# Optimization experiments

Hardware: AMD Instinct MI355X
Metric: run time of the kernel (lower is better)

## Reference

```python
import jax, jax.numpy as jnp
import numpy as np

EMBED, HID, INSIDE, OUTSIDE, EPS = 128, 64, 4, 8, 1e-5
N_NODES, N_EDGES, BATCH, SEQLEN = 16384, 262144, 64, 21


def _layernorm(x, g, b):
    m = x.mean(-1, keepdims=True)
    v = ((x - m) ** 2).mean(-1, keepdims=True)
    return (x - m) * jax.lax.rsqrt(v + EPS) * g + b


def _lstm_dir(x, Wih, Whh, bih, bhh, reverse):
    # x: [B, L, D] -> h: [B, L, HID]; PyTorch gate order i,f,g,o
    pre = jnp.einsum('bld,gd->blg', x, Wih) + bih + bhh  # [B,L,4H]
    pre = jnp.swapaxes(pre, 0, 1)  # [L,B,4H]
    h0 = jnp.zeros((x.shape[0], HID), x.dtype)

    def step(carry, xt):
        h, c = carry
        gates = xt + h @ Whh.T
        i, f, g, o = jnp.split(gates, 4, axis=-1)
        c = jax.nn.sigmoid(f) * c + jax.nn.sigmoid(i) * jnp.tanh(g)
        h = jax.nn.sigmoid(o) * jnp.tanh(c)
        return (h, c), h

    _, hs = jax.lax.scan(step, (h0, h0), pre, reverse=reverse)
    return jnp.swapaxes(hs, 0, 1)


def setup_inputs():
    key = jax.random.key(0)
    ks = jax.random.split(key, 40)
    f = jnp.float32
    N, E, B, L, D = N_NODES, N_EDGES, BATCH, SEQLEN, EMBED

    def w(k, shape, fan_in):
        return jax.random.normal(k, shape, f) * (1.0 / np.sqrt(fan_in))

    inp = {
        'x': jax.random.normal(ks[0], (N, 2561), f),
        'edge_index': jax.random.randint(ks[1], (2, E), 0, N, jnp.int32),
        'edge_attr': jax.random.normal(ks[2], (E, 3), f),
        # sorted node->graph assignment; every graph id 0..B-1 present
        'batch': ((jnp.arange(N, dtype=jnp.int32) * B) // N).astype(jnp.int32),
        'hotslice': jax.random.normal(ks[3], (B, L, 28), f),
        # randn_like noise tensors from the torch forward, made explicit inputs
        'noise_seqy': jax.random.normal(ks[4], (B, L, D), f),
        'noise_seqz': jax.random.normal(ks[5], (B, L, D), f),
        'noise_sty': jax.random.normal(ks[6], (N, D), f),
        'noise_stz': jax.random.normal(ks[7], (N, D), f),
        # AttnNN params
        'W_esm': w(ks[8], (D, 2560), 2560), 'b_esm': jnp.zeros((D,), f),
        'W_node': w(ks[9], (D, D + 1), D + 1), 'b_node': jnp.zeros((D,), f),
        'W_seq': w(ks[10], (D, 28), 28), 'b_seq': jnp.zeros((D,), f),
        # SeqStructBlock params
        'ln_seq_g': jnp.ones((D,), f), 'ln_seq_b': jnp.zeros((D,), f),
        'ln_st_g': jnp.ones((D,), f), 'ln_st_b': jnp.zeros((D,), f),
        'W_in': w(ks[11], (D, 2 * D + 3), 2 * D + 3), 'b_in': jnp.zeros((D,), f),
        'W_out': w(ks[12], (D, 2 * D + 3), 2 * D + 3), 'b_out': jnp.zeros((D,), f),
        'Wih_f': w(ks[13], (4 * HID, D), HID), 'Whh_f': w(ks[14], (4 * HID, HID), HID),
        'bih_f': jnp.zeros((4 * HID,), f), 'bhh_f': jnp.zeros((4 * HID,), f),
        'Wih_b': w(ks[15], (4 * HID, D), HID), 'Whh_b': w(ks[16], (4 * HID, HID), HID),
        'bih_b': jnp.zeros((4 * HID,), f), 'bhh_b': jnp.zeros((4 * HID,), f),
        # BatchNorm1d (eval mode: running stats)
        'bn_g': jnp.ones((D,), f), 'bn_b': jnp.zeros((D,), f),
        'bn_rm': jnp.zeros((D,), f), 'bn_rv': jnp.ones((D,), f),
    }
    return inp


def reference(x, edge_index, edge_attr, batch, hotslice,
              noise_seqy, noise_seqz, noise_sty, noise_stz,
              W_esm, b_esm, W_node, b_node, W_seq, b_seq,
              ln_seq_g, ln_seq_b, ln_st_g, ln_st_b,
              W_in, b_in, W_out, b_out,
              Wih_f, Whh_f, bih_f, bhh_f, Wih_b, Whh_b, bih_b, bhh_b,
              bn_g, bn_b, bn_rm, bn_rv):
    N = x.shape[0]
    B = hotslice.shape[0]
    src, dst = edge_index[0, 0::2], edge_index[1, 0::2]
    ea_in, ea_out = edge_attr[1::2], edge_attr[0::2]

    def ss(seq, struct):
        # bidirectional LSTM + residual + LayerNorm (dropout = identity, eval)
        hf = _lstm_dir(seq, Wih_f, Whh_f, bih_f, bhh_f, False)
        hb = _lstm_dir(seq, Wih_b, Whh_b, bih_b, bhh_b, True)
        seq = _layernorm(seq + jnp.concatenate([hf, hb], -1), ln_seq_g, ln_seq_b)
        sn = struct
        fs, fd = sn[src], sn[dst]  # [E/2, 128] gathers
        gin = jax.nn.sigmoid(jnp.concatenate([fs, fd, ea_in], -1) @ W_in.T + b_in)
        struct = struct + jax.ops.segment_sum(gin * fd, src, num_segments=N)
        gout = jax.nn.sigmoid(jnp.concatenate([fs, fd, ea_out], -1) @ W_out.T + b_out)
        struct = struct + jax.ops.segment_sum(gout * fs, dst, num_segments=N)
        return seq, _layernorm(struct, ln_st_g, ln_st_b)

    seq0 = hotslice @ W_seq.T + b_seq                       # [B,L,128]
    esm = x[:, 1:] @ W_esm.T + b_esm                        # [N,128]
    struct0 = jnp.concatenate([esm, x[:, :1]], -1) @ W_node.T + b_node  # [N,128]

    def outer(carry):
        sy, sz, ty, tz = carry

        def inner(c, _):
            szc, tzc = c
            return ss(seq0 + sy + szc, struct0 + ty + tzc), None

        (sz, tz), _ = jax.lax.scan(inner, (sz, tz), None, length=INSIDE)
        sy, ty = ss(sy + sz, ty + tz)
        return (sy, sz, ty, tz)

    carry = (noise_seqy, noise_seqz, noise_sty, noise_stz)
    carry, _ = jax.lax.scan(lambda c, _: (outer(c), None), carry, None,
                            length=OUTSIDE - 1)
    sy, sz, ty, tz = outer(carry)

    # middleSelect picks the first node of each consecutive batch run;
    # batch is sorted with every graph id present -> run starts via searchsorted
    starts = jnp.searchsorted(batch, jnp.arange(B, dtype=batch.dtype))
    feat = sy[:, 10, :] + ty[starts]                        # [B,128]
    # BatchNorm1d, eval mode (running stats)
    return (feat - bn_rm) * jax.lax.rsqrt(bn_rv + EPS) * bn_g + bn_b
```

## Files before the change

kernel.cpp:

```cpp
#include <hip/hip_runtime.h>
#include <hip/hip_fp16.h>
#include <math.h>

#define D 128
#define G4 256
#define LSEQ 21
#define EPSF 1e-5f

typedef unsigned short u16;
typedef __attribute__((ext_vector_type(8))) short bf16x8;
typedef __attribute__((ext_vector_type(4))) float f32x4;
typedef __attribute__((ext_vector_type(2))) unsigned u32x2;
typedef __attribute__((ext_vector_type(4))) unsigned u32x4;

#define MFMA16(a,b,c) __builtin_amdgcn_mfma_f32_16x16x32_bf16(a,b,c,0,0,0)

__device__ __forceinline__ float sigf(float x){ return 1.0f/(1.0f+__expf(-x)); }
__device__ __forceinline__ u16 f2bf(float x){
  unsigned u = __float_as_uint(x);
  return (u16)((u + 0x7FFFu + ((u>>16)&1u)) >> 16);
}
__device__ __forceinline__ float bf2f(u16 h){ return __uint_as_float(((unsigned)h)<<16); }
__device__ __forceinline__ unsigned pack_h2(float a, float b){
  __half2 h = __floats2half2_rn(a, b);
  return *(unsigned*)&h;
}
__device__ __forceinline__ float2 unpack_h2(unsigned u){
  __half2 h = *(__half2*)&u;
  return __half22float2(h);
}
__device__ __forceinline__ u16 f2h(float v){ __half h = __float2half(v); return *(u16*)&h; }

__device__ __forceinline__ void edge_acc(u32x4 a, uint2 g, bool valid,
                                         float2 po2, float2 w0, float2 w1, float2 w2,
                                         float& ax, float& ay){
  float e0=__uint_as_float(a.y), e1=__uint_as_float(a.z), e2=__uint_as_float(a.w);
  float2 ps0 = unpack_h2(g.x);
  float2 ps1 = unpack_h2(g.y);
  float gx = po2.x + ps0.x + e0*w0.x + e1*w1.x + e2*w2.x;
  float gy = po2.y + ps1.x + e0*w0.y + e1*w1.y + e2*w2.y;
  float mm = valid ? 1.f : 0.f;
  ax = fmaf(ps0.y*mm, sigf(gx), ax);
  ay = fmaf(ps1.y*mm, sigf(gy), ay);
}

__global__ void k_misc(int* __restrict__ starts, const int* __restrict__ batch, int N, int Bb,
                       float* __restrict__ WEin, float* __restrict__ WEout,
                       const float* __restrict__ W_in, const float* __restrict__ W_out,
                       float* __restrict__ bsum_f, float* __restrict__ bsum_b,
                       const float* __restrict__ bih_f, const float* __restrict__ bhh_f,
                       const float* __restrict__ bih_b, const float* __restrict__ bhh_b){
  int tid = threadIdx.x;
  if (tid < Bb){
    int lo = 0, hi = N;
    while (lo < hi){ int m = (lo+hi)>>1; if (batch[m] < tid) lo = m+1; else hi = m; }
    starts[tid] = lo;
  }
  for (int i = tid; i < 384; i += 256){
    int t = i >> 7, j = i & 127;
    WEin [i] = W_in [(size_t)j*259 + 256 + t];
    WEout[i] = W_out[(size_t)j*259 + 256 + t];
  }
  if (tid < 256){
    bsum_f[tid] = bih_f[tid] + bhh_f[tid];
    bsum_b[tid] = bih_b[tid] + bhh_b[tid];
  }
}

__global__ void k_packB(u16* __restrict__ PB4h, u16* __restrict__ PB4l,
                        u16* __restrict__ PBnh, u16* __restrict__ PBnl,
                        u16* __restrict__ PBEh, u16* __restrict__ PBEl,
                        const float* __restrict__ W_in, const float* __restrict__ W_out,
                        const float* __restrict__ W_node, const float* __restrict__ W_esm){
  int idx = blockIdx.x*256 + threadIdx.x;
  if (idx < 65536){
    int j = idx&7, l=(idx>>3)&63, q=idx>>9;
    int ks = q&3, nt = q>>2;
    int c = nt*16 + (l&15);
    int k = ks*32 + ((l>>4)<<3) + j;
    float v;
    if (c < 128)      v = W_in [(size_t)c*259 + k];
    else if (c < 256) v = W_in [(size_t)(c-128)*259 + 128 + k];
    else if (c < 384) v = W_out[(size_t)(c-256)*259 + k];
    else              v = W_out[(size_t)(c-384)*259 + 128 + k];
    u16 h = f2bf(v);
    PB4h[idx] = h; PB4l[idx] = f2bf(v - bf2f(h));
  } else if (idx < 65536 + 16384){
    int p = idx - 65536;
    int j = p&7, l=(p>>3)&63, q=p>>9;
    int ks = q&3, nt = q>>2;
    int c = nt*16 + (l&15);
    int k = ks*32 + ((l>>4)<<3) + j;
    float v = W_node[(size_t)c*129 + k];
    u16 h = f2bf(v);
    PBnh[p] = h; PBnl[p] = f2bf(v - bf2f(h));
  } else if (idx < 65536 + 16384 + 327680){
    int p = idx - 81920;
    int j = p&7, l=(p>>3)&63, q=p>>9;
    int ks = q%80, nt = q/80;
    int c = nt*16 + (l&15);
    int k = ks*32 + ((l>>4)<<3) + j;
    float v = W_esm[(size_t)c*2560 + k];
    u16 h = f2bf(v);
    PBEh[p] = h; PBEl[p] = f2bf(v - bf2f(h));
  }
}

__global__ void k_seq0(float* __restrict__ seq0, const float* __restrict__ hot,
                       const float* __restrict__ W_seq, const float* __restrict__ b_seq){
  int row = blockIdx.x, j = threadIdx.x;
  const float* h = hot + (size_t)row*28;
  const float* w = W_seq + (size_t)j*28;
  float acc = b_seq[j];
  #pragma unroll
  for (int k = 0; k < 28; k++) acc += h[k]*w[k];
  seq0[(size_t)row*D + j] = acc;
}

__global__ __launch_bounds__(256) void k_esm2(float* __restrict__ struct0, const float* __restrict__ x,
    const u16* __restrict__ PBEh, const u16* __restrict__ PBEl,
    const u16* __restrict__ PBnh, const u16* __restrict__ PBnl,
    const float* __restrict__ b_esm, const float* __restrict__ W_node,
    const float* __restrict__ b_node){
  __shared__ union {
    struct { u16 xh[32*72], xl[32*72]; } p1;
    struct { u16 Ah[32*136], Al[32*136]; } p2;
  } uu;
  __shared__ float esmF[32*132];
  int tid = threadIdx.x;
  int r0 = blockIdx.x*32;
  int w = tid>>6, l = tid&63;
  f32x4 acc[2][2];
  #pragma unroll
  for (int a=0;a<2;a++)
    #pragma unroll
    for (int b=0;b<2;b++) acc[a][b] = (f32x4){0.f,0.f,0.f,0.f};

  float xv[8];
  int rr = tid >> 5, k2i = tid & 31;
  #pragma unroll
  for (int q = 0; q < 4; q++){
    const float* src = x + (size_t)(r0+rr+8*q)*2561 + 1 + k2i*2;
    xv[2*q]   = src[0];
    xv[2*q+1] = src[1];
  }
  for (int kc = 0; kc < 2560; kc += 64){
    __syncthreads();
    unsigned* xh32 = (unsigned*)uu.p1.xh;
    unsigned* xl32 = (unsigned*)uu.p1.xl;
    #pragma unroll
    for (int q = 0; q < 4; q++){
      float v0 = xv[2*q], v1 = xv[2*q+1];
      u16 h0 = f2bf(v0), h1 = f2bf(v1);
      u16 l0 = f2bf(v0 - bf2f(h0)), l1 = f2bf(v1 - bf2f(h1));
      int r = rr + 8*q;
      xh32[r*36 + k2i] = (unsigned)h0 | ((unsigned)h1 << 16);
      xl32[r*36 + k2i] = (unsigned)l0 | ((unsigned)l1 << 16);
    }
    __syncthreads();
    if (kc + 64 < 2560){
      #pragma unroll
      for (int q = 0; q < 4; q++){
        const float* src = x + (size_t)(r0+rr+8*q)*2561 + 1 + kc + 64 + k2i*2;
        xv[2*q]   = src[0];
        xv[2*q+1] = src[1];
      }
    }
    #pragma unroll
    for (int ks = 0; ks < 2; ks++){
      bf16x8 ah[2], al[2];
      #pragma unroll
      for (int rt = 0; rt < 2; rt++){
        int row = rt*16 + (l&15);
        int k = ks*32 + ((l>>4)<<3);
        ah[rt] = *(const bf16x8*)&uu.p1.xh[row*72 + k];
        al[rt] = *(const bf16x8*)&uu.p1.xl[row*72 + k];
      }
      int ksg = (kc>>5) + ks;
      #pragma unroll
      for (int ctl = 0; ctl < 2; ctl++){
        int nt = w*2 + ctl;
        bf16x8 bh = *(const bf16x8*)&PBEh[((size_t)(nt*80 + ksg)*64 + l)*8];
        bf16x8 bl = *(const bf16x8*)&PBEl[((size_t)(nt*80 + ksg)*64 + l)*8];
        #pragma unroll
        for (int rt = 0; rt < 2; rt++){
          acc[rt][ctl] = MFMA16(ah[rt], bh, acc[rt][ctl]);
          acc[rt][ctl] = MFMA16(al[rt], bh, acc[rt][ctl]);
          acc[rt][ctl] = MFMA16(ah[rt], bl, acc[rt][ctl]);
        }
      }
    }
  }
  __syncthreads();
  int cq = l & 15, rqb = (l>>4)*4;
  #pragma unroll
  for (int ctl = 0; ctl < 2; ctl++){
    int coln = (w*2+ctl)*16 + cq;
    float be = b_esm[coln];
    #pragma unroll
    for (int rt = 0; rt < 2; rt++)
      #pragma unroll
      for (int r = 0; r < 4; r++)
        esmF[(rt*16+rqb+r)*132 + coln] = acc[rt][ctl][r] + be;
  }
  __syncthreads();
  {
    unsigned* Ah32 = (unsigned*)uu.p2.Ah;
    unsigned* Al32 = (unsigned*)uu.p2.Al;
    int rr2 = tid >> 6, k2 = tid & 63;
    #pragma unroll
    for (int q = 0; q < 8; q++){
      int r = rr2 + 4*q;
      float v0 = esmF[r*132 + k2*2];
      float v1 = esmF[r*132 + k2*2 + 1];
      u16 h0 = f2bf(v0), h1 = f2bf(v1);
      u16 l0 = f2bf(v0 - bf2f(h0)), l1 = f2bf(v1 - bf2f(h1));
      Ah32[r*68 + k2] = (unsigned)h0 | ((unsigned)h1 << 16);
      Al32[r*68 + k2] = (unsigned)l0 | ((unsigned)l1 << 16);
    }
  }
  __syncthreads();
  f32x4 acc2[2][2];
  #pragma unroll
  for (int a=0;a<2;a++)
    #pragma unroll
    for (int b=0;b<2;b++) acc2[a][b] = (f32x4){0.f,0.f,0.f,0.f};
  #pragma unroll
  for (int ks = 0; ks < 4; ks++){
    bf16x8 ah[2], al[2];
    #pragma unroll
    for (int rt = 0; rt < 2; rt++){
      int row = rt*16 + (l&15);
      int k = ks*32 + ((l>>4)<<3);
      ah[rt] = *(const bf16x8*)&uu.p2.Ah[row*136 + k];
      al[rt] = *(const bf16x8*)&uu.p2.Al[row*136 + k];
    }
    #pragma unroll
    for (int ctl = 0; ctl < 2; ctl++){
      int nt = w*2 + ctl;
      bf16x8 bh = *(const bf16x8*)&PBnh[((size_t)(nt*4 + ks)*64 + l)*8];
      bf16x8 bl = *(const bf16x8*)&PBnl[((size_t)(nt*4 + ks)*64 + l)*8];
      #pragma unroll
      for (int rt = 0; rt < 2; rt++){
        acc2[rt][ctl] = MFMA16(ah[rt], bh, acc2[rt][ctl]);
        acc2[rt][ctl] = MFMA16(al[rt], bh, acc2[rt][ctl]);
        acc2[rt][ctl] = MFMA16(ah[rt], bl, acc2[rt][ctl]);
      }
    }
  }
  #pragma unroll
  for (int ctl = 0; ctl < 2; ctl++){
    int col = (w*2+ctl)*16 + cq;
    float wl = W_node[(size_t)col*129 + 128];
    float bn = b_node[col];
    #pragma unroll
    for (int rt = 0; rt < 2; rt++)
      #pragma unroll
      for (int r = 0; r < 4; r++){
        int row = r0 + rt*16 + rqb + r;
        float x0 = x[(size_t)row*2561];
        struct0[(size_t)row*D + col] = acc2[rt][ctl][r] + x0*wl + bn;
      }
  }
}

__global__ void k_zero2(int* a, int* b, int n){
  int i = blockIdx.x*blockDim.x + threadIdx.x;
  if (i < n){ a[i] = 0; b[i] = 0; }
}
__global__ void k_count(int* cnt_s, int* cnt_d, const int* __restrict__ ei, int E2){
  int e = blockIdx.x*blockDim.x + threadIdx.x;
  if (e < E2){
    atomicAdd(&cnt_s[ei[2*e]], 1);
    atomicAdd(&cnt_d[ei[2*E2 + 2*e]], 1);
  }
}
__global__ __launch_bounds__(1024) void k_scan(const int* __restrict__ cnt, int* __restrict__ offs, int n){
  __shared__ int sh[1024];
  __shared__ int sbase;
  int tid = threadIdx.x;
  if (tid == 0) sbase = 0;
  __syncthreads();
  for (int chunk = 0; chunk < n; chunk += 1024){
    int v = (chunk+tid < n) ? cnt[chunk+tid] : 0;
    sh[tid] = v;
    __syncthreads();
    for (int off = 1; off < 1024; off <<= 1){
      int t = (tid >= off) ? sh[tid-off] : 0;
      __syncthreads();
      sh[tid] += t;
      __syncthreads();
    }
    if (chunk+tid < n) offs[chunk+tid] = sbase + sh[tid] - v;
    __syncthreads();
    if (tid == 0) sbase += sh[1023];
    __syncthreads();
  }
  if (tid == 0) offs[n] = sbase;
}
__global__ void k_copy2(int* cur_s, const int* offs_s, int* cur_d, const int* offs_d, int n){
  int i = blockIdx.x*blockDim.x + threadIdx.x;
  if (i < n){ cur_s[i] = offs_s[i]; cur_d[i] = offs_d[i]; }
}
__global__ void k_fill(const int* __restrict__ ei, const float* __restrict__ eattr, int E2,
                       int* cur_s, int4* __restrict__ adj_s,
                       int* cur_d, int4* __restrict__ adj_d){
  int e = blockIdx.x*blockDim.x + threadIdx.x;
  if (e >= E2) return;
  int s = ei[2*e];
  int d = ei[2*E2 + 2*e];
  const float* ein  = eattr + (size_t)(2*e+1)*3;
  const float* eout = eattr + (size_t)(2*e)*3;
  int ps = atomicAdd(&cur_s[s], 1);
  adj_s[ps] = make_int4(d, __float_as_int(ein[0]),  __float_as_int(ein[1]),  __float_as_int(ein[2]));
  int pd = atomicAdd(&cur_d[d], 1);
  adj_d[pd] = make_int4(s, __float_as_int(eout[0]), __float_as_int(eout[1]), __float_as_int(eout[2]));
}
__global__ void k_pad(int4* __restrict__ adj_s, int4* __restrict__ adj_d, int E2){
  int t = threadIdx.x;
  if (t < 8){
    adj_s[E2+t] = make_int4(0,0,0,0);
    adj_d[E2+t] = make_int4(0,0,0,0);
  }
}

__global__ __launch_bounds__(256) void k_A(
  const float* __restrict__ s0t, const float* __restrict__ ty, const float* __restrict__ tz,
  float* __restrict__ struct_in,
  const u16* __restrict__ PB4h, const u16* __restrict__ PB4l,
  unsigned* __restrict__ G_in, unsigned* __restrict__ G_out,
  unsigned* __restrict__ PownPk,
  const float* __restrict__ b_in, const float* __restrict__ b_out,
  const float* __restrict__ s0s, const float* __restrict__ sy, const float* __restrict__ sz,
  float* __restrict__ seq_in, float* __restrict__ pre_f, float* __restrict__ pre_b,
  const float* __restrict__ Wih_f, const float* __restrict__ Wih_b,
  const float* __restrict__ bsum_f, const float* __restrict__ bsum_b,
  int N, int Bb)
{
  __shared__ union {
    struct { u16 Ah[32*136], Al[32*136]; float Sf[32*132]; } m;
    float sh[LSEQ*128];
  } u;
  int tid = threadIdx.x;
  if ((int)blockIdx.x >= Bb){
    int r0 = (blockIdx.x - Bb)*32;
    const float4* ty4 = (const float4*)(ty + (size_t)r0*D);
    const float4* tz4 = (const float4*)(tz + (size_t)r0*D);
    const float4* s04 = s0t ? (const float4*)(s0t + (size_t)r0*D) : nullptr;
    float4* si4 = (float4*)(struct_in + (size_t)r0*D);
    #pragma unroll
    for (int q = 0; q < 4; q++){
      int i = tid + 256*q;
      int r = i >> 5, k4 = i & 31;
      float4 v = ty4[i];
      float4 z = tz4[i];
      v.x += z.x; v.y += z.y; v.z += z.z; v.w += z.w;
      if (s04){ float4 s = s04[i]; v.x += s.x; v.y += s.y; v.z += s.z; v.w += s.w; }
      si4[i] = v;
      u16 h0 = f2bf(v.x), h1 = f2bf(v.y), h2 = f2bf(v.z), h3 = f2bf(v.w);
      *(ushort4*)&u.m.Ah[r*136 + k4*4] = make_ushort4(h0,h1,h2,h3);
      *(ushort4*)&u.m.Al[r*136 + k4*4] = make_ushort4(
          f2bf(v.x - bf2f(h0)), f2bf(v.y - bf2f(h1)),
          f2bf(v.z - bf2f(h2)), f2bf(v.w - bf2f(h3)));
      *(float4*)&u.m.Sf[r*132 + k4*4] = v;
    }
    __syncthreads();
    int w = tid >> 6, l = tid & 63;
    f32x4 acc[2][8];
    #pragma unroll
    for (int a=0;a<2;a++)
      #pragma unroll
      for (int b=0;b<8;b++) acc[a][b] = (f32x4){0.f,0.f,0.f,0.f};
    #pragma unroll
    for (int ks = 0; ks < 4; ks++){
      bf16x8 ah[2], al[2];
      #pragma unroll
      for (int rt = 0; rt < 2; rt++){
        int row = rt*16 + (l&15);
        int k = ks*32 + ((l>>4)<<3);
        ah[rt] = *(const bf16x8*)&u.m.Ah[row*136 + k];
        al[rt] = *(const bf16x8*)&u.m.Al[row*136 + k];
      }
      #pragma unroll
      for (int ct = 0; ct < 8; ct++){
        int nt = w*8 + ct;
        bf16x8 bh = *(const bf16x8*)&PB4h[((size_t)(nt*4 + ks)*64 + l)*8];
        bf16x8 bl = *(const bf16x8*)&PB4l[((size_t)(nt*4 + ks)*64 + l)*8];
        #pragma unroll
        for (int rt = 0; rt < 2; rt++){
          acc[rt][ct] = MFMA16(ah[rt], bh, acc[rt][ct]);
          acc[rt][ct] = MFMA16(al[rt], bh, acc[rt][ct]);
          acc[rt][ct] = MFMA16(ah[rt], bl, acc[rt][ct]);
        }
      }
    }
    __syncthreads();
    unsigned* stg = (unsigned*)u.m.Ah;
    u16* stg16 = (u16*)u.m.Ah;
    int cq = l & 15, rqb = (l>>4)*4;
    if (w == 1){
      #pragma unroll
      for (int ct = 0; ct < 8; ct++){
        int coln = ct*16 + cq;
        #pragma unroll
        for (int rt = 0; rt < 2; rt++){
          #pragma unroll
          for (int r = 0; r < 4; r++){
            int lr = rt*16 + rqb + r;
            stg[lr*128 + coln] = pack_h2(acc[rt][ct][r], u.m.Sf[lr*132 + coln]);
          }
        }
      }
    }
    __syncthreads();
    {
      uint4* dst = (uint4*)(G_in + (size_t)r0*D);
      const uint4* src = (const uint4*)stg;
      #pragma unroll
      for (int q = 0; q < 4; q++) dst[tid + 256*q] = src[tid + 256*q];
    }
    __syncthreads();
    if (w == 2){
      #pragma unroll
      for (int ct = 0; ct < 8; ct++){
        int coln = ct*16 + cq;
        #pragma unroll
        for (int rt = 0; rt < 2; rt++){
          #pragma unroll
          for (int r = 0; r < 4; r++){
            int lr = rt*16 + rqb + r;
            stg[lr*128 + coln] = pack_h2(acc[rt][ct][r], u.m.Sf[lr*132 + coln]);
          }
        }
      }
    }
    __syncthreads();
    {
      uint4* dst = (uint4*)(G_out + (size_t)r0*D);
      const uint4* src = (const uint4*)stg;
      #pragma unroll
      for (int q = 0; q < 4; q++) dst[tid + 256*q] = src[tid + 256*q];
    }
    __syncthreads();
    if (w == 0 || w == 3){
      const float* bb = (w == 0) ? b_in : b_out;
      int half = (w == 0) ? 0 : 1;
      #pragma unroll
      for (int ct = 0; ct < 8; ct++){
        int coln = ct*16 + cq;
        float bc = bb[coln];
        #pragma unroll
        for (int rt = 0; rt < 2; rt++){
          #pragma unroll
          for (int r = 0; r < 4; r++){
            int lr = rt*16 + rqb + r;
            stg16[(lr*128 + coln)*2 + half] = f2h(acc[rt][ct][r] + bc);
          }
        }
      }
    }
    __syncthreads();
    {
      uint4* dst = (uint4*)(PownPk + (size_t)r0*D);
      const uint4* src = (const uint4*)stg;
      #pragma unroll
      for (int q = 0; q < 4; q++) dst[tid + 256*q] = src[tid + 256*q];
    }
  } else {
    int b = blockIdx.x;
    for (int idx = tid; idx < LSEQ*128; idx += 256){
      size_t off = (size_t)b*LSEQ*128 + idx;
      float v = sy[off] + sz[off];
      if (s0s) v += s0s[off];
      u.sh[idx] = v;
      seq_in[off] = v;
    }
    __syncthreads();
    int g = tid;
    float accf[LSEQ], accb[LSEQ];
    float bf = bsum_f[g], bb = bsum_b[g];
    #pragma unroll
    for (int l = 0; l < LSEQ; l++){ accf[l] = bf; accb[l] = bb; }
    const float* wfp = Wih_f + (size_t)g*128;
    const float* wbp = Wih_b + (size_t)g*128;
    for (int kc = 0; kc < 128; kc += 16){
      float4 wf[4], wb[4];
      #pragma unroll
      for (int q = 0; q < 4; q++){
        wf[q] = *(const float4*)(wfp + kc + 4*q);
        wb[q] = *(const float4*)(wbp + kc + 4*q);
      }
      #pragma unroll
      for (int l = 0; l < LSEQ; l++){
        #pragma unroll
        for (int q = 0; q < 4; q++){
          float4 s4 = *(const float4*)&u.sh[l*128 + kc + 4*q];
          accf[l] += s4.x*wf[q].x + s4.y*wf[q].y + s4.z*wf[q].z + s4.w*wf[q].w;
          accb[l] += s4.x*wb[q].x + s4.y*wb[q].y + s4.z*wb[q].z + s4.w*wb[q].w;
        }
      }
    }
    for (int l = 0; l < LSEQ; l++){
      pre_f[((size_t)b*LSEQ + l)*G4 + g] = accf[l];
      pre_b[((size_t)b*LSEQ + l)*G4 + g] = accb[l];
    }
  }
}

__global__ __launch_bounds__(512) void k_B(
  const unsigned* __restrict__ G_in, const unsigned* __restrict__ G_out,
  const unsigned* __restrict__ PownPk,
  const float* __restrict__ struct_in, float* __restrict__ struct_out,
  const int* __restrict__ offs_s, const int4* __restrict__ adj_s,
  const int* __restrict__ offs_d, const int4* __restrict__ adj_d,
  const float* __restrict__ WEin, const float* __restrict__ WEout,
  const float* __restrict__ ln_st_g, const float* __restrict__ ln_st_b,
  const float* __restrict__ pre_f, const float* __restrict__ pre_b,
  const float* __restrict__ Whh_f, const float* __restrict__ Whh_b,
  const float* __restrict__ seq_in, float* __restrict__ seq_out,
  const float* __restrict__ ln_seq_g, const float* __restrict__ ln_seq_b,
  int N, int Bb)
{
  __shared__ float h_hist[2][LSEQ][64];
  __shared__ float hcur[2][64];
  __shared__ float gsh[2][G4];
  if ((int)blockIdx.x >= Bb){
    int wv = threadIdx.x >> 6, lane = threadIdx.x & 63;
    int n0 = ((blockIdx.x - Bb)*8 + wv)*4;
    const float2* WEi2 = (const float2*)WEin;
    const float2* WEo2 = (const float2*)WEout;
    float2 wi0 = WEi2[lane], wi1 = WEi2[64+lane], wi2 = WEi2[128+lane];
    float2 wo0 = WEo2[lane], wo1 = WEo2[64+lane], wo2 = WEo2[128+lane];
    float2 g2v = ((const float2*)ln_st_g)[lane], be2 = ((const float2*)ln_st_b)[lane];
    const uint2* Gi = (const uint2*)G_in;
    const uint2* Go = (const uint2*)G_out;
    #pragma unroll 1
    for (int n = n0; n < n0+4; ++n){
      u32x2 pw = *((const u32x2*)PownPk + (size_t)n*64 + lane);
      float2 pp0 = unpack_h2(pw.x), pp1 = unpack_h2(pw.y);
      float2 poI = make_float2(pp0.x, pp1.x);
      float2 poO = make_float2(pp0.y, pp1.y);
      float ax = 0.f, ay = 0.f;
      int j0 = __builtin_amdgcn_readfirstlane(offs_s[n]);
      int j1 = __builtin_amdgcn_readfirstlane(offs_s[n+1]);
      for (int jb = j0; jb < j1; jb += 4){
        int rem = j1 - jb;
        const u32x4* ap = (const u32x4*)adj_s + jb;
        u32x4 a0 = ap[0], a1 = ap[1], a2 = ap[2], a3 = ap[3];
        uint2 g0 = Gi[(size_t)a0.x*64 + lane];
        uint2 g1 = Gi[(size_t)a1.x*64 + lane];
        uint2 g2 = Gi[(size_t)a2.x*64 + lane];
        uint2 g3 = Gi[(size_t)a3.x*64 + lane];
        edge_acc(a0, g0, true,  poI, wi0, wi1, wi2, ax, ay);
        edge_acc(a1, g1, rem>1, poI, wi0, wi1, wi2, ax, ay);
        edge_acc(a2, g2, rem>2, poI, wi0, wi1, wi2, ax, ay);
        edge_acc(a3, g3, rem>3, poI, wi0, wi1, wi2, ax, ay);
      }
      j0 = __builtin_amdgcn_readfirstlane(offs_d[n]);
      j1 = __builtin_amdgcn_readfirstlane(offs_d[n+1]);
      for (int jb = j0; jb < j1; jb += 4){
        int rem = j1 - jb;
        const u32x4* ap = (const u32x4*)adj_d + jb;
        u32x4 a0 = ap[0], a1 = ap[1], a2 = ap[2], a3 = ap[3];
        uint2 g0 = Go[(size_t)a0.x*64 + lane];
        uint2 g1 = Go[(size_t)a1.x*64 + lane];
        uint2 g2 = Go[(size_t)a2.x*64 + lane];
        uint2 g3 = Go[(size_t)a3.x*64 + lane];
        edge_acc(a0, g0, true,  poO, wo0, wo1, wo2, ax, ay);
        edge_acc(a1, g1, rem>1, poO, wo0, wo1, wo2, ax, ay);
        edge_acc(a2, g2, rem>2, poO, wo0, wo1, wo2, ax, ay);
        edge_acc(a3, g3, rem>3, poO, wo0, wo1, wo2, ax, ay);
      }
      float2 sn = ((const float2*)struct_in)[(size_t)n*64 + lane];
      float vx = sn.x + ax;
      float vy = sn.y + ay;
      float s = vx+vy, sq = vx*vx + vy*vy;
      #pragma unroll
      for (int o = 32; o; o >>= 1){ s += __shfl_xor(s, o); sq += __shfl_xor(sq, o); }
      float mean = s*(1.f/128.f);
      float inv = rsqrtf(sq*(1.f/128.f) - mean*mean + EPSF);
      float2 o2;
      o2.x = (vx-mean)*inv*g2v.x + be2.x;
      o2.y = (vy-mean)*inv*g2v.y + be2.y;
      ((float2*)struct_out)[(size_t)n*64 + lane] = o2;
    }
  } else {
    int b = blockIdx.x;
    int tid = threadIdx.x;
    int dir = tid >> 8, g = tid & 255;
    const float* Whh = dir ? Whh_b : Whh_f;
    const float* pre = dir ? pre_b : pre_f;
    float w[64];
    #pragma unroll
    for (int q = 0; q < 16; q++){
      float4 t4 = *(const float4*)(Whh + (size_t)g*64 + 4*q);
      w[4*q] = t4.x; w[4*q+1] = t4.y; w[4*q+2] = t4.z; w[4*q+3] = t4.w;
    }
    float c = 0.f;
    for (int t = 0; t < LSEQ; ++t){
      int tt = dir ? (LSEQ-1-t) : t;
      float gate = pre[((size_t)b*LSEQ + tt)*G4 + g];
      if (t > 0){
        #pragma unroll
        for (int q = 0; q < 16; q++){
          float4 h4 = *(const float4*)&hcur[dir][4*q];
          gate += w[4*q]*h4.x + w[4*q+1]*h4.y + w[4*q+2]*h4.z + w[4*q+3]*h4.w;
        }
      }
      gsh[dir][g] = gate;
      __syncthreads();
      if (g < 64){
        float iv = gsh[dir][g], fv = gsh[dir][64+g], gv = gsh[dir][128+g], ov = gsh[dir][192+g];
        c = sigf(fv)*c + sigf(iv)*tanhf(gv);
        float h = sigf(ov)*tanhf(c);
        hcur[dir][g] = h;
        h_hist[dir][tt][g] = h;
      }
      __syncthreads();
    }
    int wv = tid >> 6, lane = tid & 63;
    for (int l = wv; l < LSEQ; l += 8){
      float2 sv = ((const float2*)(seq_in + ((size_t)b*LSEQ + l)*128))[lane];
      float hv0, hv1;
      if (lane < 32){ hv0 = h_hist[0][l][2*lane];    hv1 = h_hist[0][l][2*lane+1]; }
      else          { hv0 = h_hist[1][l][2*lane-64]; hv1 = h_hist[1][l][2*lane-63]; }
      float vx = sv.x + hv0, vy = sv.y + hv1;
      float s = vx+vy, sq = vx*vx + vy*vy;
      #pragma unroll
      for (int o = 32; o; o >>= 1){ s += __shfl_xor(s, o); sq += __shfl_xor(sq, o); }
      float mean = s*(1.f/128.f);
      float inv = rsqrtf(sq*(1.f/128.f) - mean*mean + EPSF);
      float2 g2 = ((const float2*)ln_seq_g)[lane], b2 = ((const float2*)ln_seq_b)[lane];
      float2 o2;
      o2.x = (vx-mean)*inv*g2.x + b2.x;
      o2.y = (vy-mean)*inv*g2.y + b2.y;
      ((float2*)(seq_out + ((size_t)b*LSEQ + l)*128))[lane] = o2;
    }
  }
}

__global__ void k_final(float* __restrict__ out, const float* __restrict__ sy,
                        const float* __restrict__ ty, const int* __restrict__ starts,
                        const float* __restrict__ g, const float* __restrict__ b,
                        const float* __restrict__ rm, const float* __restrict__ rv, int Bb){
  int i = blockIdx.x*blockDim.x + threadIdx.x;
  if (i >= Bb*D) return;
  int bb = i >> 7, d = i & 127;
  float feat = sy[((size_t)bb*LSEQ + 10)*D + d] + ty[(size_t)starts[bb]*D + d];
  out[i] = (feat - rm[d])*rsqrtf(rv[d]+EPSF)*g[d] + b[d];
}

extern "C" void kernel_launch(void* const* d_in, const int* in_sizes, int n_in,
                              void* d_out, int out_size, void* d_ws, size_t ws_size,
                              hipStream_t stream)
{
  const float* x        = (const float*)d_in[0];
  const int*   ei       = (const int*)  d_in[1];
  const float* eattr    = (const float*)d_in[2];
  const int*   batch    = (const int*)  d_in[3];
  const float* hotslice = (const float*)d_in[4];
  const float* nsy      = (const float*)d_in[5];
  const float* nsz      = (const float*)d_in[6];
  const float* nty      = (const float*)d_in[7];
  const float* ntz      = (const float*)d_in[8];
  const float* W_esm    = (const float*)d_in[9];
  const float* b_esm    = (const float*)d_in[10];
  const float* W_node   = (const float*)d_in[11];
  const float* b_node   = (const float*)d_in[12];
  const float* W_seq    = (const float*)d_in[13];
  const float* b_seq    = (const float*)d_in[14];
  const float* ln_seq_g = (const float*)d_in[15];
  const float* ln_seq_b = (const float*)d_in[16];
  const float* ln_st_g  = (const float*)d_in[17];
  const float* ln_st_b  = (const float*)d_in[18];
  const float* W_in     = (const float*)d_in[19];
  const float* b_in     = (const float*)d_in[20];
  const float* W_out    = (const float*)d_in[21];
  const float* b_out    = (const float*)d_in[22];
  const float* Wih_f    = (const float*)d_in[23];
  const float* Whh_f    = (const float*)d_in[24];
  const float* bih_f    = (const float*)d_in[25];
  const float* bhh_f    = (const float*)d_in[26];
  const float* Wih_b    = (const float*)d_in[27];
  const float* Whh_b    = (const float*)d_in[28];
  const float* bih_b    = (const float*)d_in[29];
  const float* bhh_b    = (const float*)d_in[30];
  const float* bn_g     = (const float*)d_in[31];
  const float* bn_b     = (const float*)d_in[32];
  const float* bn_rm    = (const float*)d_in[33];
  const float* bn_rv    = (const float*)d_in[34];

  const int N  = in_sizes[0] / 2561;
  const int E  = in_sizes[1] / 2;
  const int E2 = E / 2;
  const int Bb = in_sizes[4] / (LSEQ*28);
  const int BL = Bb*LSEQ;

  char* p = (char*)d_ws;
  auto alloc = [&](size_t bytes)->void*{
    void* r = (void*)p; p += (bytes + 255) & ~(size_t)255; return r;
  };
  float*    seq0      = (float*)alloc((size_t)BL*D*4);
  float*    sy        = (float*)alloc((size_t)BL*D*4);
  float*    sz        = (float*)alloc((size_t)BL*D*4);
  float*    seq_in    = (float*)alloc((size_t)BL*D*4);
  float*    pre_f     = (float*)alloc((size_t)BL*G4*4);
  float*    pre_b     = (float*)alloc((size_t)BL*G4*4);
  float*    struct0   = (float*)alloc((size_t)N*D*4);
  float*    ty        = (float*)alloc((size_t)N*D*4);
  float*    tz        = (float*)alloc((size_t)N*D*4);
  float*    struct_in = (float*)alloc((size_t)N*D*4);
  unsigned* G_in      = (unsigned*)alloc((size_t)N*D*4);
  unsigned* G_out     = (unsigned*)alloc((size_t)N*D*4);
  unsigned* PownPk    = (unsigned*)alloc((size_t)N*D*4);
  u16*      PB4h      = (u16*)alloc(65536*2);
  u16*      PB4l      = (u16*)alloc(65536*2);
  u16*      PBnh      = (u16*)alloc(16384*2);
  u16*      PBnl      = (u16*)alloc(16384*2);
  u16*      PBEh      = (u16*)alloc(327680*2);
  u16*      PBEl      = (u16*)alloc(327680*2);
  float*    WEin      = (float*)alloc(384*4);
  float*    WEout     = (float*)alloc(384*4);
  float*    bsum_f    = (float*)alloc(256*4);
  float*    bsum_b    = (float*)alloc(256*4);
  int*      starts    = (int*)alloc((size_t)Bb*4);
  int*      cnt_s     = (int*)alloc((size_t)N*4);
  int*      cnt_d     = (int*)alloc((size_t)N*4);
  int*      offs_s    = (int*)alloc((size_t)(N+1)*4);
  int*      offs_d    = (int*)alloc((size_t)(N+1)*4);
  int*      cur_s     = (int*)alloc((size_t)N*4);
  int*      cur_d     = (int*)alloc((size_t)N*4);
  int4*     adj_s     = (int4*)alloc((size_t)(E2+8)*16);
  int4*     adj_d     = (int4*)alloc((size_t)(E2+8)*16);
  (void)ws_size; (void)n_in; (void)out_size;

  hipMemcpyAsync(sy, nsy, (size_t)BL*D*4, hipMemcpyDeviceToDevice, stream);
  hipMemcpyAsync(sz, nsz, (size_t)BL*D*4, hipMemcpyDeviceToDevice, stream);
  hipMemcpyAsync(ty, nty, (size_t)N*D*4, hipMemcpyDeviceToDevice, stream);
  hipMemcpyAsync(tz, ntz, (size_t)N*D*4, hipMemcpyDeviceToDevice, stream);

  k_misc<<<1, 256, 0, stream>>>(starts, batch, N, Bb, WEin, WEout, W_in, W_out,
                                bsum_f, bsum_b, bih_f, bhh_f, bih_b, bhh_b);
  k_packB<<<1600, 256, 0, stream>>>(PB4h, PB4l, PBnh, PBnl, PBEh, PBEl,
                                    W_in, W_out, W_node, W_esm);
  k_seq0<<<BL, 128, 0, stream>>>(seq0, hotslice, W_seq, b_seq);
  k_esm2<<<N/32, 256, 0, stream>>>(struct0, x, PBEh, PBEl, PBnh, PBnl,
                                   b_esm, W_node, b_node);
  k_zero2<<<(N+255)/256, 256, 0, stream>>>(cnt_s, cnt_d, N);
  k_count<<<(E2+255)/256, 256, 0, stream>>>(cnt_s, cnt_d, ei, E2);
  k_scan<<<1, 1024, 0, stream>>>(cnt_s, offs_s, N);
  k_scan<<<1, 1024, 0, stream>>>(cnt_d, offs_d, N);
  k_copy2<<<(N+255)/256, 256, 0, stream>>>(cur_s, offs_s, cur_d, offs_d, N);
  k_fill<<<(E2+255)/256, 256, 0, stream>>>(ei, eattr, E2, cur_s, adj_s, cur_d, adj_d);
  k_pad<<<1, 64, 0, stream>>>(adj_s, adj_d, E2);

  const int NB_T1 = N/32;
  const int NB_T2 = N/32;

  for (int o = 0; o < 8; ++o){
    for (int it = 0; it < 5; ++it){
      bool inner = (it < 4);
      const float* s0s = inner ? seq0 : nullptr;
      const float* s0t = inner ? struct0 : nullptr;
      float* so = inner ? sz : sy;
      float* to = inner ? tz : ty;
      k_A<<<Bb + NB_T1, 256, 0, stream>>>(s0t, ty, tz, struct_in, PB4h, PB4l,
                                          G_in, G_out, PownPk, b_in, b_out,
                                          s0s, sy, sz, seq_in, pre_f, pre_b,
                                          Wih_f, Wih_b, bsum_f, bsum_b, N, Bb);
      k_B<<<Bb + NB_T2, 512, 0, stream>>>(G_in, G_out, PownPk, struct_in, to,
                                          offs_s, adj_s, offs_d, adj_d,
                                          WEin, WEout, ln_st_g, ln_st_b,
                                          pre_f, pre_b, Whh_f, Whh_b, seq_in, so,
                                          ln_seq_g, ln_seq_b, N, Bb);
    }
  }

  k_final<<<(Bb*D+255)/256, 256, 0, stream>>>((float*)d_out, sy, ty, starts,
                                              bn_g, bn_b, bn_rm, bn_rv, Bb);
}
```

Measured before the change: 4.360 ms.

## Move LSTM input projection into previous step's sequence block and drop struct_in buffer

The sequence half of k_A (sum of seq inputs plus Wih projection) now runs at the tail of k_B's sequence blocks for the next iteration, with one initial k_seqA launch before the loop. k_A becomes a pure structure GEMM kernel. It also stops writing the fp32 struct_in buffer, and k_B reads the residual from the half packed into G_in. The aim is to shorten k_A's critical path and cut global traffic, at the cost of more shared memory and a longer tail on the 64 sequence blocks in k_B. The residual now comes from fp16 instead of fp32, which lowers precision.

```diff
diff --git a/kernel.cpp b/kernel.cpp
--- a/kernel.cpp
+++ b/kernel.cpp
@@ -324,206 +324,211 @@
   }
 }
 
+__global__ __launch_bounds__(256) void k_seqA(
+  const float* __restrict__ s0s, const float* __restrict__ sy, const float* __restrict__ sz,
+  float* __restrict__ seq_in, float* __restrict__ pre_f, float* __restrict__ pre_b,
+  const float* __restrict__ Wih_f, const float* __restrict__ Wih_b,
+  const float* __restrict__ bsum_f, const float* __restrict__ bsum_b)
+{
+  __shared__ float sh[LSEQ*128];
+  int tid = threadIdx.x;
+  int b = blockIdx.x;
+  for (int idx = tid; idx < LSEQ*128; idx += 256){
+    size_t off = (size_t)b*LSEQ*128 + idx;
+    float v = sy[off] + sz[off];
+    if (s0s) v += s0s[off];
+    sh[idx] = v;
+    seq_in[off] = v;
+  }
+  __syncthreads();
+  int g = tid;
+  float accf[LSEQ], accb[LSEQ];
+  float bf = bsum_f[g], bb = bsum_b[g];
+  #pragma unroll
+  for (int l = 0; l < LSEQ; l++){ accf[l] = bf; accb[l] = bb; }
+  const float* wfp = Wih_f + (size_t)g*128;
+  const float* wbp = Wih_b + (size_t)g*128;
+  for (int kc = 0; kc < 128; kc += 16){
+    float4 wf[4], wb[4];
+    #pragma unroll
+    for (int q = 0; q < 4; q++){
+      wf[q] = *(const float4*)(wfp + kc + 4*q);
+      wb[q] = *(const float4*)(wbp + kc + 4*q);
+    }
+    #pragma unroll
+    for (int l = 0; l < LSEQ; l++){
+      #pragma unroll
+      for (int q = 0; q < 4; q++){
+        float4 s4 = *(const float4*)&sh[l*128 + kc + 4*q];
+        accf[l] += s4.x*wf[q].x + s4.y*wf[q].y + s4.z*wf[q].z + s4.w*wf[q].w;
+        accb[l] += s4.x*wb[q].x + s4.y*wb[q].y + s4.z*wb[q].z + s4.w*wb[q].w;
+      }
+    }
+  }
+  for (int l = 0; l < LSEQ; l++){
+    pre_f[((size_t)b*LSEQ + l)*G4 + g] = accf[l];
+    pre_b[((size_t)b*LSEQ + l)*G4 + g] = accb[l];
+  }
+}
+
 __global__ __launch_bounds__(256) void k_A(
   const float* __restrict__ s0t, const float* __restrict__ ty, const float* __restrict__ tz,
-  float* __restrict__ struct_in,
   const u16* __restrict__ PB4h, const u16* __restrict__ PB4l,
   unsigned* __restrict__ G_in, unsigned* __restrict__ G_out,
   unsigned* __restrict__ PownPk,
-  const float* __restrict__ b_in, const float* __restrict__ b_out,
-  const float* __restrict__ s0s, const float* __restrict__ sy, const float* __restrict__ sz,
-  float* __restrict__ seq_in, float* __restrict__ pre_f, float* __restrict__ pre_b,
-  const float* __restrict__ Wih_f, const float* __restrict__ Wih_b,
-  const float* __restrict__ bsum_f, const float* __restrict__ bsum_b,
-  int N, int Bb)
+  const float* __restrict__ b_in, const float* __restrict__ b_out, int N)
 {
-  __shared__ union {
-    struct { u16 Ah[32*136], Al[32*136]; float Sf[32*132]; } m;
-    float sh[LSEQ*128];
-  } u;
+  __shared__ struct { u16 Ah[32*136], Al[32*136]; float Sf[32*132]; } m;
   int tid = threadIdx.x;
-  if ((int)blockIdx.x >= Bb){
-    int r0 = (blockIdx.x - Bb)*32;
-    const float4* ty4 = (const float4*)(ty + (size_t)r0*D);
-    const float4* tz4 = (const float4*)(tz + (size_t)r0*D);
-    const float4* s04 = s0t ? (const float4*)(s0t + (size_t)r0*D) : nullptr;
-    float4* si4 = (float4*)(struct_in + (size_t)r0*D);
-    #pragma unroll
-    for (int q = 0; q < 4; q++){
-      int i = tid + 256*q;
-      int r = i >> 5, k4 = i & 31;
-      float4 v = ty4[i];
-      float4 z = tz4[i];
-      v.x += z.x; v.y += z.y; v.z += z.z; v.w += z.w;
-      if (s04){ float4 s = s04[i]; v.x += s.x; v.y += s.y; v.z += s.z; v.w += s.w; }
-      si4[i] = v;
-      u16 h0 = f2bf(v.x), h1 = f2bf(v.y), h2 = f2bf(v.z), h3 = f2bf(v.w);
-      *(ushort4*)&u.m.Ah[r*136 + k4*4] = make_ushort4(h0,h1,h2,h3);
-      *(ushort4*)&u.m.Al[r*136 + k4*4] = make_ushort4(
-          f2bf(v.x - bf2f(h0)), f2bf(v.y - bf2f(h1)),
-          f2bf(v.z - bf2f(h2)), f2bf(v.w - bf2f(h3)));
-      *(float4*)&u.m.Sf[r*132 + k4*4] = v;
-    }
-    __syncthreads();
-    int w = tid >> 6, l = tid & 63;
-    f32x4 acc[2][8];
-    #pragma unroll
-    for (int a=0;a<2;a++)
-      #pragma unroll
-      for (int b=0;b<8;b++) acc[a][b] = (f32x4){0.f,0.f,0.f,0.f};
-    #pragma unroll
-    for (int ks = 0; ks < 4; ks++){
-      bf16x8 ah[2], al[2];
+  int r0 = blockIdx.x*32;
+  const float4* ty4 = (const float4*)(ty + (size_t)r0*D);
+  const float4* tz4 = (const float4*)(tz + (size_t)r0*D);
+  const float4* s04 = s0t ? (const float4*)(s0t + (size_t)r0*D) : nullptr;
+  #pragma unroll
+  for (int q = 0; q < 4; q++){
+    int i = tid + 256*q;
+    int r = i >> 5, k4 = i & 31;
+    float4 v = ty4[i];
+    float4 z = tz4[i];
+    v.x += z.x; v.y += z.y; v.z += z.z; v.w += z.w;
+    if (s04){ float4 s = s04[i]; v.x += s.x; v.y += s.y; v.z += s.z; v.w += s.w; }
+    u16 h0 = f2bf(v.x), h1 = f2bf(v.y), h2 = f2bf(v.z), h3 = f2bf(v.w);
+    *(ushort4*)&m.Ah[r*136 + k4*4] = make_ushort4(h0,h1,h2,h3);
+    *(ushort4*)&m.Al[r*136 + k4*4] = make_ushort4(
+        f2bf(v.x - bf2f(h0)), f2bf(v.y - bf2f(h1)),
+        f2bf(v.z - bf2f(h2)), f2bf(v.w - bf2f(h3)));
+    *(float4*)&m.Sf[r*132 + k4*4] = v;
+  }
+  __syncthreads();
+  int w = tid >> 6, l = tid & 63;
+  f32x4 acc[2][8];
+  #pragma unroll
+  for (int a=0;a<2;a++)
+    #pragma unroll
+    for (int b=0;b<8;b++) acc[a][b] = (f32x4){0.f,0.f,0.f,0.f};
+  #pragma unroll
+  for (int ks = 0; ks < 4; ks++){
+    bf16x8 ah[2], al[2];
+    #pragma unroll
+    for (int rt = 0; rt < 2; rt++){
+      int row = rt*16 + (l&15);
+      int k = ks*32 + ((l>>4)<<3);
+      ah[rt] = *(const bf16x8*)&m.Ah[row*136 + k];
+      al[rt] = *(const bf16x8*)&m.Al[row*136 + k];
+    }
+    #pragma unroll
+    for (int ct = 0; ct < 8; ct++){
+      int nt = w*8 + ct;
+      bf16x8 bh = *(const bf16x8*)&PB4h[((size_t)(nt*4 + ks)*64 + l)*8];
+      bf16x8 bl = *(const bf16x8*)&PB4l[((size_t)(nt*4 + ks)*64 + l)*8];
       #pragma unroll
       for (int rt = 0; rt < 2; rt++){
-        int row = rt*16 + (l&15);
-        int k = ks*32 + ((l>>4)<<3);
-        ah[rt] = *(const bf16x8*)&u.m.Ah[row*136 + k];
-        al[rt] = *(const bf16x8*)&u.m.Al[row*136 + k];
-      }
-      #pragma unroll
-      for (int ct = 0; ct < 8; ct++){
-        int nt = w*8 + ct;
-        bf16x8 bh = *(const bf16x8*)&PB4h[((size_t)(nt*4 + ks)*64 + l)*8];
-        bf16x8 bl = *(const bf16x8*)&PB4l[((size_t)(nt*4 + ks)*64 + l)*8];
+        acc[rt][ct] = MFMA16(ah[rt], bh, acc[rt][ct]);
+        acc[rt][ct] = MFMA16(al[rt], bh, acc[rt][ct]);
+        acc[rt][ct] = MFMA16(ah[rt], bl, acc[rt][ct]);
+      }
+    }
+  }
+  __syncthreads();
+  unsigned* stg = (unsigned*)m.Ah;
+  u16* stg16 = (u16*)m.Ah;
+  int cq = l & 15, rqb = (l>>4)*4;
+  if (w == 1){
+    #pragma unroll
+    for (int ct = 0; ct < 8; ct++){
+      int coln = ct*16 + cq;
+      #pragma unroll
+      for (int rt = 0; rt < 2; rt++){
         #pragma unroll
-        for (int rt = 0; rt < 2; rt++){
-          acc[rt][ct] = MFMA16(ah[rt], bh, acc[rt][ct]);
-          acc[rt][ct] = MFMA16(al[rt], bh, acc[rt][ct]);
-          acc[rt][ct] = MFMA16(ah[rt], bl, acc[rt][ct]);
+        for (int r = 0; r < 4; r++){
+          int lr = rt*16 + rqb + r;
+          stg[lr*128 + coln] = pack_h2(acc[rt][ct][r], m.Sf[lr*132 + coln]);
         }
       }
     }
-    __syncthreads();
-    unsigned* stg = (unsigned*)u.m.Ah;
-    u16* stg16 = (u16*)u.m.Ah;
-    int cq = l & 15, rqb = (l>>4)*4;
-    if (w == 1){
-      #pragma unroll
-      for (int ct = 0; ct < 8; ct++){
-        int coln = ct*16 + cq;
+  }
+  __syncthreads();
+  {
+    uint4* dst = (uint4*)(G_in + (size_t)r0*D);
+    const uint4* src = (const uint4*)stg;
+    #pragma unroll
+    for (int q = 0; q < 4; q++) dst[tid + 256*q] = src[tid + 256*q];
+  }
+  __syncthreads();
+  if (w == 2){
+    #pragma unroll
+    for (int ct = 0; ct < 8; ct++){
+      int coln = ct*16 + cq;
+      #pragma unroll
+      for (int rt = 0; rt < 2; rt++){
         #pragma unroll
-        for (int rt = 0; rt < 2; rt++){
-          #pragma unroll
-          for (int r = 0; r < 4; r++){
-            int lr = rt*16 + rqb + r;
-            stg[lr*128 + coln] = pack_h2(acc[rt][ct][r], u.m.Sf[lr*132 + coln]);
-          }
+        for (int r = 0; r < 4; r++){
+          int lr = rt*16 + rqb + r;
+          stg[lr*128 + coln] = pack_h2(acc[rt][ct][r], m.Sf[lr*132 + coln]);
         }
       }
     }
-    __syncthreads();
-    {
-      uint4* dst = (uint4*)(G_in + (size_t)r0*D);
-      const uint4* src = (const uint4*)stg;
-      #pragma unroll
-      for (int q = 0; q < 4; q++) dst[tid + 256*q] = src[tid + 256*q];
-    }
-    __syncthreads();
-    if (w == 2){
-      #pragma unroll
-      for (int ct = 0; ct < 8; ct++){
-        int coln = ct*16 + cq;
+  }
+  __syncthreads();
+  {
+    uint4* dst = (uint4*)(G_out + (size_t)r0*D);
+    const uint4* src = (const uint4*)stg;
+    #pragma unroll
+    for (int q = 0; q < 4; q++) dst[tid + 256*q] = src[tid + 256*q];
+  }
+  __syncthreads();
+  if (w == 0 || w == 3){
+    const float* bb = (w == 0) ? b_in : b_out;
+    int half = (w == 0) ? 0 : 1;
+    #pragma unroll
+    for (int ct = 0; ct < 8; ct++){
+      int coln = ct*16 + cq;
+      float bc = bb[coln];
+      #pragma unroll
+      for (int rt = 0; rt < 2; rt++){
         #pragma unroll
-        for (int rt = 0; rt < 2; rt++){
-          #pragma unroll
-          for (int r = 0; r < 4; r++){
-            int lr = rt*16 + rqb + r;
-            stg[lr*128 + coln] = pack_h2(acc[rt][ct][r], u.m.Sf[lr*132 + coln]);
-          }
+        for (int r = 0; r < 4; r++){
+          int lr = rt*16 + rqb + r;
+          stg16[(lr*128 + coln)*2 + half] = f2h(acc[rt][ct][r] + bc);
         }
       }
     }
-    __syncthreads();
-    {
-      uint4* dst = (uint4*)(G_out + (size_t)r0*D);
-      const uint4* src = (const uint4*)stg;
-      #pragma unroll
-      for (int q = 0; q < 4; q++) dst[tid + 256*q] = src[tid + 256*q];
-    }
-    __syncthreads();
-    if (w == 0 || w == 3){
-      const float* bb = (w == 0) ? b_in : b_out;
-      int half = (w == 0) ? 0 : 1;
-      #pragma unroll
-      for (int ct = 0; ct < 8; ct++){
-        int coln = ct*16 + cq;
-        float bc = bb[coln];
-        #pragma unroll
-        for (int rt = 0; rt < 2; rt++){
-          #pragma unroll
-          for (int r = 0; r < 4; r++){
-            int lr = rt*16 + rqb + r;
-            stg16[(lr*128 + coln)*2 + half] = f2h(acc[rt][ct][r] + bc);
-          }
-        }
-      }
-    }
-    __syncthreads();
-    {
-      uint4* dst = (uint4*)(PownPk + (size_t)r0*D);
-      const uint4* src = (const uint4*)stg;
-      #pragma unroll
-      for (int q = 0; q < 4; q++) dst[tid + 256*q] = src[tid + 256*q];
-    }
-  } else {
-    int b = blockIdx.x;
-    for (int idx = tid; idx < LSEQ*128; idx += 256){
-      size_t off = (size_t)b*LSEQ*128 + idx;
-      float v = sy[off] + sz[off];
-      if (s0s) v += s0s[off];
-      u.sh[idx] = v;
-      seq_in[off] = v;
-    }
-    __syncthreads();
-    int g = tid;
-    float accf[LSEQ], accb[LSEQ];
-    float bf = bsum_f[g], bb = bsum_b[g];
-    #pragma unroll
-    for (int l = 0; l < LSEQ; l++){ accf[l] = bf; accb[l] = bb; }
-    const float* wfp = Wih_f + (size_t)g*128;
-    const float* wbp = Wih_b + (size_t)g*128;
-    for (int kc = 0; kc < 128; kc += 16){
-      float4 wf[4], wb[4];
-      #pragma unroll
-      for (int q = 0; q < 4; q++){
-        wf[q] = *(const float4*)(wfp + kc + 4*q);
-        wb[q] = *(const float4*)(wbp + kc + 4*q);
-      }
-      #pragma unroll
-      for (int l = 0; l < LSEQ; l++){
-        #pragma unroll
-        for (int q = 0; q < 4; q++){
-          float4 s4 = *(const float4*)&u.sh[l*128 + kc + 4*q];
-          accf[l] += s4.x*wf[q].x + s4.y*wf[q].y + s4.z*wf[q].z + s4.w*wf[q].w;
-          accb[l] += s4.x*wb[q].x + s4.y*wb[q].y + s4.z*wb[q].z + s4.w*wb[q].w;
-        }
-      }
-    }
-    for (int l = 0; l < LSEQ; l++){
-      pre_f[((size_t)b*LSEQ + l)*G4 + g] = accf[l];
-      pre_b[((size_t)b*LSEQ + l)*G4 + g] = accb[l];
-    }
+  }
+  __syncthreads();
+  {
+    uint4* dst = (uint4*)(PownPk + (size_t)r0*D);
+    const uint4* src = (const uint4*)stg;
+    #pragma unroll
+    for (int q = 0; q < 4; q++) dst[tid + 256*q] = src[tid + 256*q];
   }
 }
 
 __global__ __launch_bounds__(512) void k_B(
   const unsigned* __restrict__ G_in, const unsigned* __restrict__ G_out,
   const unsigned* __restrict__ PownPk,
-  const float* __restrict__ struct_in, float* __restrict__ struct_out,
+  float* __restrict__ to,
   const int* __restrict__ offs_s, const int4* __restrict__ adj_s,
   const int* __restrict__ offs_d, const int4* __restrict__ adj_d,
   const float* __restrict__ WEin, const float* __restrict__ WEout,
   const float* __restrict__ ln_st_g, const float* __restrict__ ln_st_b,
-  const float* __restrict__ pre_f, const float* __restrict__ pre_b,
+  float* pre_f, float* pre_b,
   const float* __restrict__ Whh_f, const float* __restrict__ Whh_b,
-  const float* __restrict__ seq_in, float* __restrict__ seq_out,
+  float* seq_in, float* __restrict__ so,
+  const float* __restrict__ otherS, const float* __restrict__ s0s_n,
+  const float* __restrict__ Wih_f, const float* __restrict__ Wih_b,
+  const float* __restrict__ bsum_f, const float* __restrict__ bsum_b,
   const float* __restrict__ ln_seq_g, const float* __restrict__ ln_seq_b,
-  int N, int Bb)
+  int doNext, int N, int Bb)
 {
-  __shared__ float h_hist[2][LSEQ][64];
-  __shared__ float hcur[2][64];
-  __shared__ float gsh[2][G4];
+  __shared__ union {
+    struct {
+      float h_hist[2][LSEQ][64];
+      float hcur[2][64];
+      float gsh[2][G4];
+      float soL[LSEQ*128];
+      float shG[LSEQ*128];
+    } sq;
+  } u;
   if ((int)blockIdx.x >= Bb){
     int wv = threadIdx.x >> 6, lane = threadIdx.x & 63;
     int n0 = ((blockIdx.x - Bb)*8 + wv)*4;
@@ -540,6 +545,7 @@
       float2 pp0 = unpack_h2(pw.x), pp1 = unpack_h2(pw.y);
       float2 poI = make_float2(pp0.x, pp1.x);
       float2 poO = make_float2(pp0.y, pp1.y);
+      uint2 gown = Gi[(size_t)n*64 + lane];
       float ax = 0.f, ay = 0.f;
       int j0 = __builtin_amdgcn_readfirstlane(offs_s[n]);
       int j1 = __builtin_amdgcn_readfirstlane(offs_s[n+1]);
@@ -571,9 +577,8 @@
         edge_acc(a2, g2, rem>2, poO, wo0, wo1, wo2, ax, ay);
         edge_acc(a3, g3, rem>3, poO, wo0, wo1, wo2, ax, ay);
       }
-      float2 sn = ((const float2*)struct_in)[(size_t)n*64 + lane];
-      float vx = sn.x + ax;
-      float vy = sn.y + ay;
+      float vx = unpack_h2(gown.x).y + ax;
+      float vy = unpack_h2(gown.y).y + ay;
       float s = vx+vy, sq = vx*vx + vy*vy;
       #pragma unroll
       for (int o = 32; o; o >>= 1){ s += __shfl_xor(s, o); sq += __shfl_xor(sq, o); }
@@ -582,7 +587,7 @@
       float2 o2;
       o2.x = (vx-mean)*inv*g2v.x + be2.x;
       o2.y = (vy-mean)*inv*g2v.y + be2.y;
-      ((float2*)struct_out)[(size_t)n*64 + lane] = o2;
+      ((float2*)to)[(size_t)n*64 + lane] = o2;
     }
   } else {
     int b = blockIdx.x;
@@ -603,18 +608,19 @@
       if (t > 0){
         #pragma unroll
         for (int q = 0; q < 16; q++){
-          float4 h4 = *(const float4*)&hcur[dir][4*q];
+          float4 h4 = *(const float4*)&u.sq.hcur[dir][4*q];
           gate += w[4*q]*h4.x + w[4*q+1]*h4.y + w[4*q+2]*h4.z + w[4*q+3]*h4.w;
         }
       }
-      gsh[dir][g] = gate;
+      u.sq.gsh[dir][g] = gate;
       __syncthreads();
       if (g < 64){
-        float iv = gsh[dir][g], fv = gsh[dir][64+g], gv = gsh[dir][128+g], ov = gsh[dir][192+g];
+        float iv = u.sq.gsh[dir][g], fv = u.sq.gsh[dir][64+g];
+        float gv = u.sq.gsh[dir][128+g], ov = u.sq.gsh[dir][192+g];
         c = sigf(fv)*c + sigf(iv)*tanhf(gv);
         float h = sigf(ov)*tanhf(c);
-        hcur[dir][g] = h;
-        h_hist[dir][tt][g] = h;
+        u.sq.hcur[dir][g] = h;
+        u.sq.h_hist[dir][tt][g] = h;
       }
       __syncthreads();
     }
@@ -622,8 +628,8 @@
     for (int l = wv; l < LSEQ; l += 8){
       float2 sv = ((const float2*)(seq_in + ((size_t)b*LSEQ + l)*128))[lane];
       float hv0, hv1;
-      if (lane < 32){ hv0 = h_hist[0][l][2*lane];    hv1 = h_hist[0][l][2*lane+1]; }
-      else          { hv0 = h_hist[1][l][2*lane-64]; hv1 = h_hist[1][l][2*lane-63]; }
+      if (lane < 32){ hv0 = u.sq.h_hist[0][l][2*lane];    hv1 = u.sq.h_hist[0][l][2*lane+1]; }
+      else          { hv0 = u.sq.h_hist[1][l][2*lane-64]; hv1 = u.sq.h_hist[1][l][2*lane-63]; }
       float vx = sv.x + hv0, vy = sv.y + hv1;
       float s = vx+vy, sq = vx*vx + vy*vy;
       #pragma unroll
@@ -634,7 +640,50 @@
       float2 o2;
       o2.x = (vx-mean)*inv*g2.x + b2.x;
       o2.y = (vy-mean)*inv*g2.y + b2.y;
-      ((float2*)(seq_out + ((size_t)b*LSEQ + l)*128))[lane] = o2;
+      ((float2*)(so + ((size_t)b*LSEQ + l)*128))[lane] = o2;
+      u.sq.soL[l*128 + 2*lane]     = o2.x;
+      u.sq.soL[l*128 + 2*lane + 1] = o2.y;
+    }
+    if (!doNext) return;
+    __syncthreads();
+    {
+      const float4* oS4 = (const float4*)(otherS + (size_t)b*LSEQ*128);
+      const float4* s04 = s0s_n ? (const float4*)(s0s_n + (size_t)b*LSEQ*128) : nullptr;
+      float4* gi4 = (float4*)(seq_in + (size_t)b*LSEQ*128);
+      for (int idx = tid; idx < LSEQ*32; idx += 512){
+        float4 v = *(const float4*)&u.sq.soL[idx*4];
+        float4 o = oS4[idx];
+        v.x += o.x; v.y += o.y; v.z += o.z; v.w += o.w;
+        if (s04){ float4 s0 = s04[idx]; v.x += s0.x; v.y += s0.y; v.z += s0.z; v.w += s0.w; }
+        *(float4*)&u.sq.shG[idx*4] = v;
+        gi4[idx] = v;
+      }
+    }
+    __syncthreads();
+    {
+      int g2 = tid & 255;
+      int dn = tid >> 8;
+      const float* wp = (dn ? Wih_b : Wih_f) + (size_t)g2*128;
+      float bsv = dn ? bsum_b[g2] : bsum_f[g2];
+      float accv[LSEQ];
+      #pragma unroll
+      for (int l = 0; l < LSEQ; l++) accv[l] = bsv;
+      for (int kc = 0; kc < 128; kc += 16){
+        float4 wf[4];
+        #pragma unroll
+        for (int q = 0; q < 4; q++) wf[q] = *(const float4*)(wp + kc + 4*q);
+        #pragma unroll
+        for (int l = 0; l < LSEQ; l++){
+          #pragma unroll
+          for (int q = 0; q < 4; q++){
+            float4 s4 = *(const float4*)&u.sq.shG[l*128 + kc + 4*q];
+            accv[l] += s4.x*wf[q].x + s4.y*wf[q].y + s4.z*wf[q].z + s4.w*wf[q].w;
+          }
+        }
+      }
+      float* dst = dn ? pre_b : pre_f;
+      for (int l = 0; l < LSEQ; l++)
+        dst[((size_t)b*LSEQ + l)*G4 + g2] = accv[l];
     }
   }
 }
@@ -709,7 +758,6 @@
   float*    struct0   = (float*)alloc((size_t)N*D*4);
   float*    ty        = (float*)alloc((size_t)N*D*4);
   float*    tz        = (float*)alloc((size_t)N*D*4);
-  float*    struct_in = (float*)alloc((size_t)N*D*4);
   unsigned* G_in      = (unsigned*)alloc((size_t)N*D*4);
   unsigned* G_out     = (unsigned*)alloc((size_t)N*D*4);
   unsigned* PownPk    = (unsigned*)alloc((size_t)N*D*4);
@@ -753,26 +801,31 @@
   k_copy2<<<(N+255)/256, 256, 0, stream>>>(cur_s, offs_s, cur_d, offs_d, N);
   k_fill<<<(E2+255)/256, 256, 0, stream>>>(ei, eattr, E2, cur_s, adj_s, cur_d, adj_d);
   k_pad<<<1, 64, 0, stream>>>(adj_s, adj_d, E2);
-
-  const int NB_T1 = N/32;
-  const int NB_T2 = N/32;
+  k_seqA<<<Bb, 256, 0, stream>>>(seq0, sy, sz, seq_in, pre_f, pre_b,
+                                 Wih_f, Wih_b, bsum_f, bsum_b);
+
+  const int NB = N/32;
 
   for (int o = 0; o < 8; ++o){
     for (int it = 0; it < 5; ++it){
+      int gi = o*5 + it;
       bool inner = (it < 4);
-      const float* s0s = inner ? seq0 : nullptr;
       const float* s0t = inner ? struct0 : nullptr;
-      float* so = inner ? sz : sy;
-      float* to = inner ? tz : ty;
-      k_A<<<Bb + NB_T1, 256, 0, stream>>>(s0t, ty, tz, struct_in, PB4h, PB4l,
-                                          G_in, G_out, PownPk, b_in, b_out,
-                                          s0s, sy, sz, seq_in, pre_f, pre_b,
-                                          Wih_f, Wih_b, bsum_f, bsum_b, N, Bb);
-      k_B<<<Bb + NB_T2, 512, 0, stream>>>(G_in, G_out, PownPk, struct_in, to,
-                                          offs_s, adj_s, offs_d, adj_d,
-                                          WEin, WEout, ln_st_g, ln_st_b,
-                                          pre_f, pre_b, Whh_f, Whh_b, seq_in, so,
-                                          ln_seq_g, ln_seq_b, N, Bb);
+      float* to_ = inner ? tz : ty;
+      float* so_ = inner ? sz : sy;
+      const float* otherS = inner ? sy : sz;
+      int itn = (gi+1) % 5;
+      const float* s0s_n = (itn < 4) ? seq0 : nullptr;
+      int doNext = (gi < 39) ? 1 : 0;
+      k_A<<<NB, 256, 0, stream>>>(s0t, ty, tz, PB4h, PB4l,
+                                  G_in, G_out, PownPk, b_in, b_out, N);
+      k_B<<<Bb + NB, 512, 0, stream>>>(G_in, G_out, PownPk, to_,
+                                       offs_s, adj_s, offs_d, adj_d,
+                                       WEin, WEout, ln_st_g, ln_st_b,
+                                       pre_f, pre_b, Whh_f, Whh_b,
+                                       seq_in, so_, otherS, s0s_n,
+                                       Wih_f, Wih_b, bsum_f, bsum_b,
+                                       ln_seq_g, ln_seq_b, doNext, N, Bb);
     }
   }
 
```

New measurement: 3.629 ms. 16.7% less time.
